# Performance work log

Measured on AMD Instinct MI355X. Metric: run time of the kernel, lower is better.

## Reference

```python
import jax, jax.numpy as jnp
import numpy as np

NTYPES = 2
B, N, MNEI = 4, 512, 100
M = MNEI * NTYPES          # neighbor slots = maxNeighborNum * ntypes
EMB_LAST = 100             # embedding net sizes [25, 50, 100]
FIT_H = 240
M2 = 16
RMIN, RMAX = 0.5, 6.0


def setup_inputs():
    key = jax.random.key(0)
    ks = jax.random.split(key, 24)
    r = jax.random.uniform(ks[0], (B, N, M), minval=0.6, maxval=7.0)
    v = jax.random.normal(ks[1], (B, N, M, 3))
    v = v / jnp.linalg.norm(v, axis=-1, keepdims=True)
    keep = jax.random.uniform(ks[2], (B, N, M)) < 0.7
    ImageDR = jnp.concatenate([r[..., None], r[..., None] * v], axis=-1)
    ImageDR = jnp.where(keep[..., None], ImageDR, 0.0).astype(jnp.float32)
    Imagetype_map = jax.random.randint(ks[3], (N,), 0, NTYPES)
    list_neigh = jax.random.randint(ks[4], (B, N, M), 0, N + 1)
    type_map = jnp.arange(NTYPES)
    davg = (0.01 * jax.random.normal(ks[5], (NTYPES, M, 4))).astype(jnp.float32)
    dstd = (1.0 + 0.1 * jax.random.uniform(ks[6], (NTYPES, M, 4))).astype(jnp.float32)

    def w(k, shape, fan):
        return (jax.random.normal(k, shape) / np.sqrt(fan)).astype(jnp.float32)

    def b(k, shape):
        return (0.1 * jax.random.normal(k, shape)).astype(jnp.float32)

    emb_W0 = w(ks[7], (NTYPES, NTYPES, 1, 25), 1)
    emb_b0 = b(ks[8], (NTYPES, NTYPES, 25))
    emb_W1 = w(ks[9], (NTYPES, NTYPES, 25, 50), 25)
    emb_b1 = b(ks[10], (NTYPES, NTYPES, 50))
    emb_W2 = w(ks[11], (NTYPES, NTYPES, 50, 100), 50)
    emb_b2 = b(ks[12], (NTYPES, NTYPES, 100))
    fin = M2 * EMB_LAST
    fit_W0 = w(ks[13], (NTYPES, fin, FIT_H), fin)
    fit_b0 = b(ks[14], (NTYPES, FIT_H))
    fit_W1 = w(ks[15], (NTYPES, FIT_H, FIT_H), FIT_H)
    fit_b1 = b(ks[16], (NTYPES, FIT_H))
    fit_W2 = w(ks[17], (NTYPES, FIT_H, FIT_H), FIT_H)
    fit_b2 = b(ks[18], (NTYPES, FIT_H))
    fit_W3 = w(ks[19], (NTYPES, FIT_H, 1), FIT_H)
    fit_b3 = b(ks[20], (NTYPES, 1))
    energy_shift = jnp.array([-3.37, -5.21], dtype=jnp.float32)
    return dict(list_neigh=list_neigh, Imagetype_map=Imagetype_map, type_map=type_map,
                ImageDR=ImageDR, nghost=0, davg=davg, dstd=dstd,
                emb_W0=emb_W0, emb_b0=emb_b0, emb_W1=emb_W1, emb_b1=emb_b1,
                emb_W2=emb_W2, emb_b2=emb_b2,
                fit_W0=fit_W0, fit_b0=fit_b0, fit_W1=fit_W1, fit_b1=fit_b1,
                fit_W2=fit_W2, fit_b2=fit_b2, fit_W3=fit_W3, fit_b3=fit_b3,
                energy_shift=energy_shift)


def _emb(s, W0, b0, W1, b1, W2, b2):
    # DeepPot-SE embedding net with doubling resnet connections
    h = jnp.tanh(s @ W0 + b0)                                   # [..., 25]
    h = jnp.tanh(h @ W1 + b1) + jnp.concatenate([h, h], -1)     # [..., 50]
    return jnp.tanh(h @ W2 + b2) + jnp.concatenate([h, h], -1)  # [..., 100]


def _fit(d, W0, b0, W1, b1, W2, b2, W3, b3):
    h = jnp.tanh(d @ W0 + b0)
    h = h + jnp.tanh(h @ W1 + b1)
    h = h + jnp.tanh(h @ W2 + b2)
    return h @ W3 + b3


def _forward(ImageDR, davg, dstd,
             emb_W0, emb_b0, emb_W1, emb_b1, emb_W2, emb_b2,
             fit_W0, fit_b0, fit_W1, fit_b1, fit_W2, fit_b2, fit_W3, fit_b3,
             energy_shift, Imagetype_map):
    Bsz, Nat, Mtot, _ = ImageDR.shape
    m = Mtot // NTYPES
    R = ImageDR[..., 0]
    Rsafe = jnp.where(R > 1e-5, R, 1.0)
    # smooth switching function s(r): 1/r below Rmin, polynomial taper to Rmax
    u = (R - RMIN) / (RMAX - RMIN)
    mid = (u ** 3 * (-6.0 * u * u + 15.0 * u - 10.0) + 1.0) / Rsafe
    S = jnp.where((R > 0) & (R < RMIN), 1.0 / Rsafe,
                  jnp.where((R > RMIN) & (R < RMAX), mid, 0.0))
    msk = (jnp.abs(R) > 1e-5)[..., None]
    Ri = jnp.concatenate([S[..., None],
                          jnp.where(msk, (S / Rsafe)[..., None] * ImageDR[..., 1:4], 0.0)],
                         axis=-1)                                    # [B,N,M,4] = (s, s*x/r, s*y/r, s*z/r)
    # per-center-type normalization (irregular gather of stats)
    Rn = (Ri - davg[Imagetype_map][None]) / dstd[Imagetype_map][None]
    tmask = [(Imagetype_map == i).astype(Rn.dtype)[None, :, None, None] for i in range(NTYPES)]
    xyz = jnp.zeros((Bsz, Nat, 4, EMB_LAST), Rn.dtype)
    for j in range(NTYPES):                                          # neighbor-type slice
        sl = Rn[:, :, j * m:(j + 1) * m, :]                          # [B,N,m,4]
        s = sl[..., 0:1]
        G = jnp.zeros(sl.shape[:3] + (EMB_LAST,), sl.dtype)
        for i in range(NTYPES):                                      # center type -> pair net (i, j)
            G = G + tmask[i] * _emb(s, emb_W0[i, j], emb_b0[i, j],
                                    emb_W1[i, j], emb_b1[i, j], emb_W2[i, j], emb_b2[i, j])
        xyz = xyz + jnp.einsum('bnmk,bnmc->bnkc', sl, G)
    xyz = xyz / (m * NTYPES)
    # descriptor D = (Ri^T G)^T (Ri^T G)[:, :M2], flattened -> [B,N,EMB_LAST*M2]
    D = jnp.einsum('bnkc,bnkd->bncd', xyz, xyz[..., :M2]).reshape(Bsz, Nat, -1)
    Ei = jnp.zeros((Bsz, Nat), D.dtype)
    for i in range(NTYPES):
        e = _fit(D, fit_W0[i], fit_b0[i], fit_W1[i], fit_b1[i],
                 fit_W2[i], fit_b2[i], fit_W3[i], fit_b3[i])[..., 0] + energy_shift[i]
        Ei = Ei + tmask[i][:, :, 0, 0] * e
    Etot = jnp.sum(Ei, axis=1)
    return Etot, Ei


def reference(list_neigh, Imagetype_map, type_map, ImageDR, nghost, davg, dstd,
              emb_W0, emb_b0, emb_W1, emb_b1, emb_W2, emb_b2,
              fit_W0, fit_b0, fit_W1, fit_b1, fit_W2, fit_b2, fit_W3, fit_b3,
              energy_shift):
    return _forward(ImageDR, davg, dstd,
                    emb_W0, emb_b0, emb_W1, emb_b1, emb_W2, emb_b2,
                    fit_W0, fit_b0, fit_W1, fit_b1, fit_W2, fit_b2, fit_W3, fit_b3,
                    energy_shift, Imagetype_map)
```

## Files before the change

kernel.cpp:

```cpp
#include <hip/hip_runtime.h>
#include <math.h>

#define NT 2
#define BSZ 4
#define NAT 512
#define NATOMS 2048
#define NNEI 200
#define EMB 100
#define FITH 240
#define DDIM 1600
#define TBK 1024

#define BIAS_F  16
#define W3C_F   (BIAS_F + 3 * 512)
#define PERM_I  2064
#define CNT_I   (PERM_I + 2048)
#define USH_BYTE 16512
#define TBL_U   0
#define W0T_U   409600
#define W1T_U   (W0T_U + 819200)
#define W2T_U   (W1T_U + 262144)
#define D_U     (W2T_U + 262144)
#define H0_U    (D_U + 3276800)
#define H1_U    (H0_U + 1048576)
#define USH_END (H1_U + 1048576)
#define WS_NEED ((size_t)USH_BYTE + (size_t)USH_END * 2)

#define N_W0 819200
#define N_W1 262144
#define N_W2 262144
#define N_B  1536
#define N_W3 512
#define N_EI 2048
#define N_WT (N_W0 + N_W1 + N_W2 + N_B + N_W3 + N_EI)
#define WT_BLK ((N_WT + 255) / 256)
#define TB_BLK 512

typedef short s8v __attribute__((ext_vector_type(8)));
typedef float f4v __attribute__((ext_vector_type(4)));

__device__ __forceinline__ float ftanh(float x) {
    float ax = fabsf(x);
    float e = __expf(2.0f * ax);
    float t = 1.0f - __fdividef(2.0f, e + 1.0f);
    return (x < 0.0f) ? -t : t;
}
__device__ __forceinline__ unsigned short f2bf(float f) {
    unsigned u = __float_as_uint(f);
    u += 0x7FFFu + ((u >> 16) & 1u);
    return (unsigned short)(u >> 16);
}
__device__ __forceinline__ float bf2f(unsigned short s) {
    return __uint_as_float(((unsigned)s) << 16);
}
__device__ __forceinline__ float calc_S(float R) {
    float Rsafe = (R > 1e-5f) ? R : 1.0f;
    float u = (R - 0.5f) * (1.0f / 5.5f);
    float uu = u * u;
    float mid = (u * uu * (-6.0f * uu + 15.0f * u - 10.0f) + 1.0f) / Rsafe;
    float S = 0.0f;
    if (R > 0.0f && R < 0.5f)      S = 1.0f / Rsafe;
    else if (R > 0.5f && R < 6.0f) S = mid;
    return S;
}

__global__ void __launch_bounds__(256) prep_kernel(
    const float* __restrict__ fW0, const float* __restrict__ fW1,
    const float* __restrict__ fW2,
    const float* __restrict__ fb0, const float* __restrict__ fb1,
    const float* __restrict__ fb2,
    const float* __restrict__ fW3, const float* __restrict__ fb3,
    const float* __restrict__ eshift,
    const float* __restrict__ davg, const float* __restrict__ dstd,
    const float* __restrict__ eW0, const float* __restrict__ eb0,
    const float* __restrict__ eW1, const float* __restrict__ eb1,
    const float* __restrict__ eW2, const float* __restrict__ eb2,
    const int* __restrict__ itype,
    float* __restrict__ ws, float* __restrict__ out)
{
    __shared__ float los[100], his[100];
    __shared__ float rng[2];
    __shared__ float h0s[8][25];
    __shared__ float h1s[8][50];
    __shared__ int pcnt, poff0, poff1;
    const int tid = threadIdx.x;
    int bxg = blockIdx.x;
    unsigned short* u0 = (unsigned short*)((char*)ws + USH_BYTE);

    if (bxg < WT_BLK) {
        int id = bxg * 256 + tid;
        if (id < N_W0) {
            int n = id / 1600, k = id - n * 1600;
            float v = 0.0f;
            if (n < 240)                  v = fW0[(size_t)k * 240 + n];
            else if (n >= 256 && n < 496) v = fW0[(size_t)(1600 + k) * 240 + (n - 256)];
            u0[W0T_U + id] = f2bf(v);
            return;
        }
        id -= N_W0;
        if (id < N_W1) {
            int n = id / 512, k = id - n * 512;
            float v = 0.0f;
            if (n < 240 && k < 240)       v = fW1[(size_t)k * 240 + n];
            else if (n >= 256 && n < 496 && k >= 256 && k < 496)
                                          v = fW1[(size_t)(240 + (k - 256)) * 240 + (n - 256)];
            u0[W1T_U + id] = f2bf(v);
            return;
        }
        id -= N_W1;
        if (id < N_W2) {
            int n = id / 512, k = id - n * 512;
            float v = 0.0f;
            if (n < 240 && k < 240)       v = fW2[(size_t)k * 240 + n];
            else if (n >= 256 && n < 496 && k >= 256 && k < 496)
                                          v = fW2[(size_t)(240 + (k - 256)) * 240 + (n - 256)];
            u0[W2T_U + id] = f2bf(v);
            return;
        }
        id -= N_W2;
        if (id < N_B) {
            int l = id / 512, n = id - l * 512;
            const float* fb = (l == 0) ? fb0 : (l == 1) ? fb1 : fb2;
            float v = 0.0f;
            if (n < 240)                  v = fb[n];
            else if (n >= 256 && n < 496) v = fb[240 + (n - 256)];
            ws[BIAS_F + l * 512 + n] = v;
            return;
        }
        id -= N_B;
        if (id < N_W3) {
            int n = id;
            float v = 0.0f;
            if (n < 240)                  v = fW3[n];
            else if (n >= 256 && n < 496) v = fW3[240 + (n - 256)];
            ws[W3C_F + n] = v;
            return;
        }
        id -= N_W3;
        if (id < N_EI) {
            int t = itype[id & (NAT - 1)];
            out[4 + id] = fb3[t] + eshift[t];
        }
        return;
    }
    bxg -= WT_BLK;
    if (bxg < TB_BLK) {
        const int nid = bxg >> 7;
        const int kb  = (bxg & 127) * 8;
        const int t = nid >> 1, j = nid & 1;
        if (tid < 100) {
            int m = j * 100 + tid;
            float av = davg[(t * NNEI + m) * 4];
            float sd = dstd[(t * NNEI + m) * 4];
            float inv = __fdividef(1.0f, sd);
            float a = (0.0f - av) * inv;
            float b = (2.0f - av) * inv;
            los[tid] = fminf(a, b);
            his[tid] = fmaxf(a, b);
        }
        __syncthreads();
        if (tid == 0) {
            float lo = los[0], hi = his[0];
            for (int i = 1; i < 100; ++i) { lo = fminf(lo, los[i]); hi = fmaxf(hi, his[i]); }
            rng[0] = lo; rng[1] = hi - lo;
            if (kb == 0) {
                ws[nid * 2] = lo;
                ws[nid * 2 + 1] = (float)(TBK - 1) / (hi - lo);
            }
        }
        __syncthreads();
        const float smin = rng[0], span = rng[1];
        const float* W0 = eW0 + nid * 25;
        const float* B0 = eb0 + nid * 25;
        if (tid < 200) {
            int q = tid / 25, a = tid % 25;
            float s = smin + span * ((float)(kb + q) * (1.0f / (TBK - 1)));
            h0s[q][a] = ftanh(fmaf(s, W0[a], B0[a]));
        }
        __syncthreads();
        const float* W1 = eW1 + nid * 1250;
        const float* B1 = eb1 + nid * 50;
        for (int idx = tid; idx < 400; idx += 256) {
            int q = idx / 50, cc = idx % 50;
            float acc = B1[cc];
#pragma unroll
            for (int a = 0; a < 25; ++a) acc = fmaf(h0s[q][a], W1[a * 50 + cc], acc);
            h1s[q][cc] = ftanh(acc) + h0s[q][(cc < 25) ? cc : cc - 25];
        }
        __syncthreads();
        const float* W2 = eW2 + nid * 5000;
        const float* B2 = eb2 + nid * 100;
        unsigned short* tblu = u0 + TBL_U;
        for (int idx = tid; idx < 800; idx += 256) {
            int q = idx / 100, c = idx % 100;
            float acc = B2[c];
#pragma unroll
            for (int a = 0; a < 50; ++a) acc = fmaf(h1s[q][a], W2[a * 100 + c], acc);
            float g = ftanh(acc) + h1s[q][(c < 50) ? c : c - 50];
            tblu[(size_t)(nid * TBK + kb + q) * 100 + c] = f2bf(g);
        }
        return;
    }
    if (tid == 0) { pcnt = 0; poff0 = 0; poff1 = 0; }
    __syncthreads();
    int* wsi = (int*)ws;
    int local0 = 0;
    for (int i = tid; i < NATOMS; i += 256) local0 += (itype[i & (NAT - 1)] == 0);
    atomicAdd(&pcnt, local0);
    __syncthreads();
    const int c0 = pcnt;
    for (int i = tid; i < NATOMS; i += 256) {
        int t = itype[i & (NAT - 1)];
        int pos = (t == 0) ? atomicAdd(&poff0, 1) : (c0 + atomicAdd(&poff1, 1));
        wsi[PERM_I + pos] = i;
    }
    if (tid == 0) { wsi[CNT_I] = c0; wsi[CNT_I + 1] = NATOMS - c0; }
}

__global__ void __launch_bounds__(128) embed_kernel(
    const int* __restrict__ itype, const float* __restrict__ imagedr,
    const float* __restrict__ davg, const float* __restrict__ dstd,
    float* __restrict__ ws)
{
    __shared__ __align__(16) float4 srn[NNEI];
    __shared__ float sx[NNEI];
    __shared__ float part[2][400];
    const int atom = blockIdx.x;
    const int n = atom & (NAT - 1);
    const int tid = threadIdx.x;
    const int t = itype[n];
    unsigned short* u0 = (unsigned short*)((char*)ws + USH_BYTE);

    const float sm0 = ws[(t * 2 + 0) * 2], sc0 = ws[(t * 2 + 0) * 2 + 1];
    const float sm1 = ws[(t * 2 + 1) * 2], sc1 = ws[(t * 2 + 1) * 2 + 1];

    for (int m = tid; m < NNEI; m += 128) {
        float4 dr = ((const float4*)imagedr)[(size_t)atom * NNEI + m];
        float R = dr.x;
        float S = calc_S(R);
        float Rsafe = (R > 1e-5f) ? R : 1.0f;
        float sr = (fabsf(R) > 1e-5f) ? (S / Rsafe) : 0.0f;
        float4 av = ((const float4*)davg)[t * NNEI + m];
        float4 sd = ((const float4*)dstd)[t * NNEI + m];
        float4 rv;
        rv.x = (S         - av.x) / sd.x;
        rv.y = (sr * dr.y - av.y) / sd.y;
        rv.z = (sr * dr.z - av.z) / sd.z;
        rv.w = (sr * dr.w - av.w) / sd.w;
        srn[m] = rv;
        float smin = (m >= 100) ? sm1 : sm0;
        float scal = (m >= 100) ? sc1 : sc0;
        sx[m] = fminf(fmaxf((rv.x - smin) * scal, 0.0f), (float)(TBK - 2) + 0.9999f);
    }
    __syncthreads();

    const int w = tid >> 6, lane = tid & 63;
    const unsigned short* T = u0 + TBL_U + (size_t)(t * 2 + w) * TBK * EMB;
    const bool hi = (lane < 36);
    float xA0 = 0, xA1 = 0, xA2 = 0, xA3 = 0;
    float xB0 = 0, xB1 = 0, xB2 = 0, xB3 = 0;
#pragma unroll 4
    for (int mi = 0; mi < 100; ++mi) {
        int m = w * 100 + mi;
        float4 rv = srn[m];
        float x = sx[m];
        int i = (int)x;
        float f = x - (float)i;
        const unsigned short* Tr = T + (size_t)i * EMB;
        float g0 = bf2f(Tr[lane]);
        float g1 = bf2f(Tr[EMB + lane]);
        float g = fmaf(f, g1 - g0, g0);
        xA0 = fmaf(rv.x, g, xA0); xA1 = fmaf(rv.y, g, xA1);
        xA2 = fmaf(rv.z, g, xA2); xA3 = fmaf(rv.w, g, xA3);
        if (hi) {
            float h0v = bf2f(Tr[64 + lane]);
            float h1v = bf2f(Tr[EMB + 64 + lane]);
            float g2 = fmaf(f, h1v - h0v, h0v);
            xB0 = fmaf(rv.x, g2, xB0); xB1 = fmaf(rv.y, g2, xB1);
            xB2 = fmaf(rv.z, g2, xB2); xB3 = fmaf(rv.w, g2, xB3);
        }
    }
    part[w][0 * 100 + lane] = xA0; part[w][1 * 100 + lane] = xA1;
    part[w][2 * 100 + lane] = xA2; part[w][3 * 100 + lane] = xA3;
    if (hi) {
        part[w][0 * 100 + 64 + lane] = xB0; part[w][1 * 100 + 64 + lane] = xB1;
        part[w][2 * 100 + 64 + lane] = xB2; part[w][3 * 100 + 64 + lane] = xB3;
    }
    __syncthreads();
    const float inv = 1.0f / 200.0f;
    for (int idx = tid; idx < 400; idx += 128)
        part[0][idx] = (part[0][idx] + part[1][idx]) * inv;
    __syncthreads();
    unsigned short* Drow = u0 + D_U + (size_t)atom * DDIM;
    const float* xt = part[0];
    for (int idx = tid; idx < DDIM; idx += 128) {
        int c = idx >> 4, d = idx & 15;
        float s = xt[c] * xt[d] + xt[100 + c] * xt[100 + d]
                + xt[200 + c] * xt[200 + d] + xt[300 + c] * xt[300 + d];
        Drow[idx] = f2bf(s);
    }
}

__global__ void __launch_bounds__(128) gemm0_kernel(
    const unsigned short* __restrict__ A,
    const unsigned short* __restrict__ BT,
    const float* __restrict__ bias,
    const int* __restrict__ wsi,
    unsigned short* __restrict__ Out)
{
    __shared__ float lred[64][17];
    const int z = blockIdx.z;
    const int cnt = wsi[CNT_I + z];
    const int my = blockIdx.y;
    if (my * 16 >= cnt) return;
    const int base = z ? wsi[CNT_I] : 0;
    const int tid = threadIdx.x;
    const int w = tid >> 6, lane = tid & 63;
    const int mr = lane & 15, q = lane >> 4;
    const int n0 = z * 256 + blockIdx.x * 64;
    const int m0 = my * 16;
    const int arow = wsi[PERM_I + base + min(m0 + mr, cnt - 1)];
    const unsigned short* Ap = A  + (size_t)arow * DDIM + w * 800 + q * 8;
    const unsigned short* Bp = BT + (size_t)(n0 + mr) * DDIM + w * 800 + q * 8;

    f4v a0 = {0,0,0,0}, a1 = {0,0,0,0}, a2 = {0,0,0,0}, a3 = {0,0,0,0};
#pragma unroll 5
    for (int kt = 0; kt < 25; ++kt) {
        s8v av = *(const s8v*)(Ap + kt * 32);
        s8v b0 = *(const s8v*)(Bp + kt * 32);
        s8v b1 = *(const s8v*)(Bp + 16 * DDIM + kt * 32);
        s8v b2 = *(const s8v*)(Bp + 32 * DDIM + kt * 32);
        s8v b3 = *(const s8v*)(Bp + 48 * DDIM + kt * 32);
        a0 = __builtin_amdgcn_mfma_f32_16x16x32_bf16(av, b0, a0, 0, 0, 0);
        a1 = __builtin_amdgcn_mfma_f32_16x16x32_bf16(av, b1, a1, 0, 0, 0);
        a2 = __builtin_amdgcn_mfma_f32_16x16x32_bf16(av, b2, a2, 0, 0, 0);
        a3 = __builtin_amdgcn_mfma_f32_16x16x32_bf16(av, b3, a3, 0, 0, 0);
    }
    if (w == 1) {
#pragma unroll
        for (int r = 0; r < 4; ++r) {
            lred[lane][r]      = a0[r];
            lred[lane][4 + r]  = a1[r];
            lred[lane][8 + r]  = a2[r];
            lred[lane][12 + r] = a3[r];
        }
    }
    __syncthreads();
    if (w == 0) {
#pragma unroll
        for (int j = 0; j < 4; ++j) {
            const int col = n0 + j * 16 + mr;
            const float bv = bias[col];
            f4v* ap = (j == 0) ? &a0 : (j == 1) ? &a1 : (j == 2) ? &a2 : &a3;
#pragma unroll
            for (int r = 0; r < 4; ++r) {
                int rl = m0 + q * 4 + r;
                if (rl < cnt) {
                    int orow = wsi[PERM_I + base + rl];
                    float s = (*ap)[r] + lred[lane][j * 4 + r] + bv;
                    Out[(size_t)orow * 512 + col] = f2bf(ftanh(s));
                }
            }
        }
    }
}

__global__ void __launch_bounds__(64) gemmr_kernel(
    const unsigned short* __restrict__ A, const unsigned short* __restrict__ BT,
    const float* __restrict__ bias, const unsigned short* __restrict__ Res,
    unsigned short* __restrict__ Out,
    const float* __restrict__ w3c, const int* __restrict__ wsi,
    float* __restrict__ out, int mode)
{
    const int z = blockIdx.z;
    const int cnt = wsi[CNT_I + z];
    const int my = blockIdx.y;
    if (my * 16 >= cnt) return;
    const int base = z ? wsi[CNT_I] : 0;
    const int lane = threadIdx.x;
    const int mr = lane & 15, q = lane >> 4;
    const int n0 = z * 256 + blockIdx.x * 64;
    const int k0 = z * 256;
    const int m0 = my * 16;
    const int arow = wsi[PERM_I + base + min(m0 + mr, cnt - 1)];
    const unsigned short* Ap = A  + (size_t)arow * 512 + k0 + q * 8;
    const unsigned short* Bp = BT + (size_t)(n0 + mr) * 512 + k0 + q * 8;

    f4v a0 = {0,0,0,0}, a1 = {0,0,0,0}, a2 = {0,0,0,0}, a3 = {0,0,0,0};
#pragma unroll
    for (int kt = 0; kt < 8; ++kt) {
        s8v av = *(const s8v*)(Ap + kt * 32);
        s8v b0 = *(const s8v*)(Bp + kt * 32);
        s8v b1 = *(const s8v*)(Bp + 16 * 512 + kt * 32);
        s8v b2 = *(const s8v*)(Bp + 32 * 512 + kt * 32);
        s8v b3 = *(const s8v*)(Bp + 48 * 512 + kt * 32);
        a0 = __builtin_amdgcn_mfma_f32_16x16x32_bf16(av, b0, a0, 0, 0, 0);
        a1 = __builtin_amdgcn_mfma_f32_16x16x32_bf16(av, b1, a1, 0, 0, 0);
        a2 = __builtin_amdgcn_mfma_f32_16x16x32_bf16(av, b2, a2, 0, 0, 0);
        a3 = __builtin_amdgcn_mfma_f32_16x16x32_bf16(av, b3, a3, 0, 0, 0);
    }
    const float bv0 = bias[n0 + mr],      bv1 = bias[n0 + 16 + mr];
    const float bv2 = bias[n0 + 32 + mr], bv3 = bias[n0 + 48 + mr];
    if (mode == 1) {
#pragma unroll
        for (int r = 0; r < 4; ++r) {
            int rl = m0 + q * 4 + r;
            if (rl < cnt) {
                int orow = wsi[PERM_I + base + rl];
                size_t b_ = (size_t)orow * 512 + n0 + mr;
                Out[b_]      = f2bf(bf2f(Res[b_])      + ftanh(a0[r] + bv0));
                Out[b_ + 16] = f2bf(bf2f(Res[b_ + 16]) + ftanh(a1[r] + bv1));
                Out[b_ + 32] = f2bf(bf2f(Res[b_ + 32]) + ftanh(a2[r] + bv2));
                Out[b_ + 48] = f2bf(bf2f(Res[b_ + 48]) + ftanh(a3[r] + bv3));
            }
        }
    } else {
        const float w30 = w3c[n0 + mr],      w31 = w3c[n0 + 16 + mr];
        const float w32 = w3c[n0 + 32 + mr], w33 = w3c[n0 + 48 + mr];
#pragma unroll
        for (int r = 0; r < 4; ++r) {
            int rl = m0 + q * 4 + r;
            if (rl < cnt) {
                int orow = wsi[PERM_I + base + rl];
                size_t b_ = (size_t)orow * 512 + n0 + mr;
                float p = (bf2f(Res[b_])      + ftanh(a0[r] + bv0)) * w30
                        + (bf2f(Res[b_ + 16]) + ftanh(a1[r] + bv1)) * w31
                        + (bf2f(Res[b_ + 32]) + ftanh(a2[r] + bv2)) * w32
                        + (bf2f(Res[b_ + 48]) + ftanh(a3[r] + bv3)) * w33;
                p += __shfl_xor(p, 1, 16);
                p += __shfl_xor(p, 2, 16);
                p += __shfl_xor(p, 4, 16);
                p += __shfl_xor(p, 8, 16);
                if (mr == 0) atomicAdd(&out[4 + orow], p);
            }
        }
    }
}

__global__ void etot_kernel(float* __restrict__ out) {
    const int b = blockIdx.x;
    float s = 0.0f;
    for (int n = threadIdx.x; n < NAT; n += 256) s += out[4 + b * NAT + n];
#pragma unroll
    for (int off = 32; off > 0; off >>= 1) s += __shfl_down(s, off, 64);
    __shared__ float rr[4];
    if ((threadIdx.x & 63) == 0) rr[threadIdx.x >> 6] = s;
    __syncthreads();
    if (threadIdx.x == 0) out[b] = rr[0] + rr[1] + rr[2] + rr[3];
}

__global__ void dp_atom_kernel(
    const int* __restrict__ itype, const float* __restrict__ imagedr,
    const float* __restrict__ davg, const float* __restrict__ dstd,
    const float* __restrict__ eW0, const float* __restrict__ eb0,
    const float* __restrict__ eW1, const float* __restrict__ eb1,
    const float* __restrict__ eW2, const float* __restrict__ eb2,
    const float* __restrict__ fW0, const float* __restrict__ fb0,
    const float* __restrict__ fW1, const float* __restrict__ fb1,
    const float* __restrict__ fW2, const float* __restrict__ fb2,
    const float* __restrict__ fW3, const float* __restrict__ fb3,
    const float* __restrict__ eshift, float* __restrict__ out)
{
    __shared__ __align__(16) float4 rn4[NNEI];
    __shared__ __align__(16) float  xyz[4 * EMB];
    __shared__ __align__(16) float  h0s[100 * 25];
    __shared__ __align__(16) float  smem[100 * 52];
    const int atom = blockIdx.x;
    const int n = atom & (NAT - 1);
    const int tid = threadIdx.x;
    const int t = itype[n];
    for (int m = tid; m < NNEI; m += 256) {
        float4 dr = ((const float4*)imagedr)[(size_t)atom * NNEI + m];
        float R = dr.x;
        float S = calc_S(R);
        float Rsafe = (R > 1e-5f) ? R : 1.0f;
        float sr = (fabsf(R) > 1e-5f) ? (S / Rsafe) : 0.0f;
        float4 av = ((const float4*)davg)[t * NNEI + m];
        float4 sd = ((const float4*)dstd)[t * NNEI + m];
        float4 rv;
        rv.x = (S - av.x) / sd.x; rv.y = (sr * dr.y - av.y) / sd.y;
        rv.z = (sr * dr.z - av.z) / sd.z; rv.w = (sr * dr.w - av.w) / sd.w;
        rn4[m] = rv;
    }
    const int c = tid & 127; const int mh = tid >> 7;
    float xp0 = 0, xp1 = 0, xp2 = 0, xp3 = 0;
    for (int j = 0; j < NT; ++j) {
        const int wb = t * NT + j;
        const float* W0 = eW0 + wb * 25; const float* B0 = eb0 + wb * 25;
        const float* W1 = eW1 + wb * 1250; const float* B1 = eb1 + wb * 50;
        const float* W2 = eW2 + wb * 5000; const float* B2 = eb2 + wb * 100;
        __syncthreads();
        for (int idx = tid; idx < 2500; idx += 256) {
            int m = idx / 25, a = idx - m * 25;
            h0s[idx] = ftanh(fmaf(rn4[j * 100 + m].x, W0[a], B0[a]));
        }
        __syncthreads();
        for (int idx = tid; idx < 5000; idx += 256) {
            int m = idx / 50, cc = idx - m * 50;
            const float* h0m = h0s + m * 25;
            float acc = B1[cc];
#pragma unroll
            for (int a = 0; a < 25; ++a) acc = fmaf(h0m[a], W1[a * 50 + cc], acc);
            smem[m * 52 + cc] = ftanh(acc) + h0m[(cc < 25) ? cc : cc - 25];
        }
        for (int idx = tid; idx < 200; idx += 256)
            smem[(idx >> 1) * 52 + 50 + (idx & 1)] = 0.0f;
        __syncthreads();
        if (c < EMB) {
            float w2c[52];
#pragma unroll
            for (int a = 0; a < 50; ++a) w2c[a] = W2[a * EMB + c];
            w2c[50] = 0; w2c[51] = 0;
            const float bc = B2[c];
            const int sk = (c < 50) ? c : c - 50;
            for (int i = 0; i < 50; ++i) {
                int m = mh * 50 + i;
                const float* h1m = smem + m * 52;
                float acc = bc;
#pragma unroll
                for (int q = 0; q < 13; ++q) {
                    float4 hv = ((const float4*)h1m)[q];
                    acc = fmaf(hv.x, w2c[4 * q], acc); acc = fmaf(hv.y, w2c[4 * q + 1], acc);
                    acc = fmaf(hv.z, w2c[4 * q + 2], acc); acc = fmaf(hv.w, w2c[4 * q + 3], acc);
                }
                float g = ftanh(acc) + h1m[sk];
                float4 rm = rn4[j * 100 + m];
                xp0 = fmaf(rm.x, g, xp0); xp1 = fmaf(rm.y, g, xp1);
                xp2 = fmaf(rm.z, g, xp2); xp3 = fmaf(rm.w, g, xp3);
            }
        }
    }
    __syncthreads();
    const float inv = 1.0f / 200.0f;
    if (mh == 0 && c < EMB) {
        xyz[c] = xp0 * inv; xyz[EMB + c] = xp1 * inv;
        xyz[2 * EMB + c] = xp2 * inv; xyz[3 * EMB + c] = xp3 * inv;
    }
    __syncthreads();
    if (mh == 1 && c < EMB) {
        xyz[c] += xp0 * inv; xyz[EMB + c] += xp1 * inv;
        xyz[2 * EMB + c] += xp2 * inv; xyz[3 * EMB + c] += xp3 * inv;
    }
    __syncthreads();
    float* Dld = smem;
    for (int idx = tid; idx < DDIM; idx += 256) {
        int cc = idx >> 4, d = idx & 15;
        Dld[idx] = xyz[cc] * xyz[d] + xyz[EMB + cc] * xyz[EMB + d]
                 + xyz[2 * EMB + cc] * xyz[2 * EMB + d] + xyz[3 * EMB + cc] * xyz[3 * EMB + d];
    }
    __syncthreads();
    float* hA = smem + DDIM; float* hB = hA + FITH; float* h2 = hB + FITH; float* red = h2 + FITH;
    if (tid < FITH) {
        const float* W = fW0 + (size_t)t * DDIM * FITH;
        float acc = fb0[t * FITH + tid];
        for (int f = 0; f < DDIM; f += 4) {
            float4 dv = *(const float4*)(Dld + f);
            acc = fmaf(dv.x, W[f * FITH + tid], acc); acc = fmaf(dv.y, W[(f + 1) * FITH + tid], acc);
            acc = fmaf(dv.z, W[(f + 2) * FITH + tid], acc); acc = fmaf(dv.w, W[(f + 3) * FITH + tid], acc);
        }
        hA[tid] = ftanh(acc);
    }
    __syncthreads();
    if (tid < FITH) {
        const float* W = fW1 + t * FITH * FITH;
        float acc = fb1[t * FITH + tid];
        for (int f = 0; f < FITH; f += 4) {
            float4 hv = *(const float4*)(hA + f);
            acc = fmaf(hv.x, W[f * FITH + tid], acc); acc = fmaf(hv.y, W[(f + 1) * FITH + tid], acc);
            acc = fmaf(hv.z, W[(f + 2) * FITH + tid], acc); acc = fmaf(hv.w, W[(f + 3) * FITH + tid], acc);
        }
        hB[tid] = hA[tid] + ftanh(acc);
    }
    __syncthreads();
    if (tid < FITH) {
        const float* W = fW2 + t * FITH * FITH;
        float acc = fb2[t * FITH + tid];
        for (int f = 0; f < FITH; f += 4) {
            float4 hv = *(const float4*)(hB + f);
            acc = fmaf(hv.x, W[f * FITH + tid], acc); acc = fmaf(hv.y, W[(f + 1) * FITH + tid], acc);
            acc = fmaf(hv.z, W[(f + 2) * FITH + tid], acc); acc = fmaf(hv.w, W[(f + 3) * FITH + tid], acc);
        }
        h2[tid] = hB[tid] + ftanh(acc);
    }
    __syncthreads();
    float p = (tid < FITH) ? h2[tid] * fW3[t * FITH + tid] : 0.0f;
#pragma unroll
    for (int off = 32; off > 0; off >>= 1) p += __shfl_down(p, off, 64);
    if ((tid & 63) == 0) red[tid >> 6] = p;
    __syncthreads();
    if (tid == 0) out[4 + atom] = red[0] + red[1] + red[2] + red[3] + fb3[t] + eshift[t];
}

extern "C" void kernel_launch(void* const* d_in, const int* in_sizes, int n_in,
                              void* d_out, int out_size, void* d_ws, size_t ws_size,
                              hipStream_t stream) {
    const int*   itype   = (const int*)  d_in[1];
    const float* imagedr = (const float*)d_in[3];
    const float* davg    = (const float*)d_in[5];
    const float* dstd    = (const float*)d_in[6];
    const float* eW0     = (const float*)d_in[7];
    const float* eb0     = (const float*)d_in[8];
    const float* eW1     = (const float*)d_in[9];
    const float* eb1     = (const float*)d_in[10];
    const float* eW2     = (const float*)d_in[11];
    const float* eb2     = (const float*)d_in[12];
    const float* fW0     = (const float*)d_in[13];
    const float* fb0     = (const float*)d_in[14];
    const float* fW1     = (const float*)d_in[15];
    const float* fb1     = (const float*)d_in[16];
    const float* fW2     = (const float*)d_in[17];
    const float* fb2     = (const float*)d_in[18];
    const float* fW3     = (const float*)d_in[19];
    const float* fb3     = (const float*)d_in[20];
    const float* eshift  = (const float*)d_in[21];
    float* out = (float*)d_out;
    float* ws  = (float*)d_ws;

    if (ws_size >= WS_NEED) {
        unsigned short* u0 = (unsigned short*)((char*)ws + USH_BYTE);
        const int* wsi = (const int*)ws;
        prep_kernel<<<WT_BLK + TB_BLK + 1, 256, 0, stream>>>(
            fW0, fW1, fW2, fb0, fb1, fb2, fW3, fb3, eshift,
            davg, dstd, eW0, eb0, eW1, eb1, eW2, eb2, itype, ws, out);
        embed_kernel<<<NATOMS, 128, 0, stream>>>(itype, imagedr, davg, dstd, ws);
        gemm0_kernel<<<dim3(4, 128, 2), 128, 0, stream>>>(
            u0 + D_U, u0 + W0T_U, ws + BIAS_F, wsi, u0 + H0_U);
        gemmr_kernel<<<dim3(4, 128, 2), 64, 0, stream>>>(
            u0 + H0_U, u0 + W1T_U, ws + BIAS_F + 512, u0 + H0_U, u0 + H1_U,
            nullptr, wsi, nullptr, 1);
        gemmr_kernel<<<dim3(4, 128, 2), 64, 0, stream>>>(
            u0 + H1_U, u0 + W2T_U, ws + BIAS_F + 1024, u0 + H1_U, nullptr,
            ws + W3C_F, wsi, out, 2);
        etot_kernel<<<BSZ, 256, 0, stream>>>(out);
    } else {
        dp_atom_kernel<<<NATOMS, 256, 0, stream>>>(itype, imagedr, davg, dstd,
            eW0, eb0, eW1, eb1, eW2, eb2,
            fW0, fb0, fW1, fb1, fW2, fb2, fW3, fb3, eshift, out);
        etot_kernel<<<BSZ, 256, 0, stream>>>(out);
    }
}
```

Before: 191.4 us.

## Fuse three fitting-net GEMM kernels into one kernel with LDS-resident hidden activations

Replaces the gemm0 kernel and the two gemmr launches with a single fit_kernel. Each 512-thread block owns 16 atom rows and all 256 output columns of its type, and keeps the hidden activations in padded shared memory between layers. This removes two kernel launches, the global-memory round trips for H0/H1, and the atomicAdd on energies, which become one plain add per row. In exchange each layer's K is split across two wave halves, which adds block-wide syncs and LDS reductions, and the grid shrinks to 256 blocks, so parallelism drops.

```diff
diff --git a/kernel.cpp b/kernel.cpp
--- a/kernel.cpp
+++ b/kernel.cpp
@@ -35,6 +35,8 @@
 #define N_WT (N_W0 + N_W1 + N_W2 + N_B + N_W3 + N_EI)
 #define WT_BLK ((N_WT + 255) / 256)
 #define TB_BLK 512
+
+#define HPAD 264
 
 typedef short s8v __attribute__((ext_vector_type(8)));
 typedef float f4v __attribute__((ext_vector_type(4)));
@@ -301,138 +303,159 @@
     }
 }
 
-__global__ void __launch_bounds__(128) gemm0_kernel(
+__device__ __forceinline__ void fit_gemm256(
+    const unsigned short* Hsrc, const unsigned short* Bp,
+    int h, int mr, int q, f4v acc[4])
+{
+#pragma unroll
+    for (int kt = 0; kt < 4; ++kt) {
+        s8v av = *(const s8v*)((const char*)Hsrc
+                 + (size_t)mr * (HPAD * 2) + h * 256 + q * 16 + kt * 64);
+#pragma unroll
+        for (int j = 0; j < 4; ++j) {
+            s8v b = *(const s8v*)(Bp + j * 16 * 512 + kt * 32);
+            acc[j] = __builtin_amdgcn_mfma_f32_16x16x32_bf16(av, b, acc[j], 0, 0, 0);
+        }
+    }
+}
+
+__global__ void __launch_bounds__(512) fit_kernel(
     const unsigned short* __restrict__ A,
-    const unsigned short* __restrict__ BT,
-    const float* __restrict__ bias,
+    const unsigned short* __restrict__ W0T,
+    const unsigned short* __restrict__ W1T,
+    const unsigned short* __restrict__ W2T,
+    const float* __restrict__ biases,
+    const float* __restrict__ w3c,
     const int* __restrict__ wsi,
-    unsigned short* __restrict__ Out)
+    float* __restrict__ out)
 {
-    __shared__ float lred[64][17];
-    const int z = blockIdx.z;
+    __shared__ float lred[4][64][17];
+    __shared__ unsigned short Hs0[16 * HPAD];
+    __shared__ unsigned short Hs1[16 * HPAD];
+    __shared__ float red2[16][4];
+
+    const int z = blockIdx.y;
     const int cnt = wsi[CNT_I + z];
-    const int my = blockIdx.y;
+    const int my = blockIdx.x;
     if (my * 16 >= cnt) return;
     const int base = z ? wsi[CNT_I] : 0;
     const int tid = threadIdx.x;
     const int w = tid >> 6, lane = tid & 63;
     const int mr = lane & 15, q = lane >> 4;
-    const int n0 = z * 256 + blockIdx.x * 64;
+    const int wc = w & 3, h = w >> 2;
+    const int n0 = z * 256 + wc * 64;
     const int m0 = my * 16;
     const int arow = wsi[PERM_I + base + min(m0 + mr, cnt - 1)];
-    const unsigned short* Ap = A  + (size_t)arow * DDIM + w * 800 + q * 8;
-    const unsigned short* Bp = BT + (size_t)(n0 + mr) * DDIM + w * 800 + q * 8;
-
-    f4v a0 = {0,0,0,0}, a1 = {0,0,0,0}, a2 = {0,0,0,0}, a3 = {0,0,0,0};
+
+    {
+        const unsigned short* Ap = A   + (size_t)arow * DDIM + h * 800 + q * 8;
+        const unsigned short* Bp = W0T + (size_t)(n0 + mr) * DDIM + h * 800 + q * 8;
+        f4v a0 = {0,0,0,0}, a1 = {0,0,0,0}, a2 = {0,0,0,0}, a3 = {0,0,0,0};
 #pragma unroll 5
-    for (int kt = 0; kt < 25; ++kt) {
-        s8v av = *(const s8v*)(Ap + kt * 32);
-        s8v b0 = *(const s8v*)(Bp + kt * 32);
-        s8v b1 = *(const s8v*)(Bp + 16 * DDIM + kt * 32);
-        s8v b2 = *(const s8v*)(Bp + 32 * DDIM + kt * 32);
-        s8v b3 = *(const s8v*)(Bp + 48 * DDIM + kt * 32);
-        a0 = __builtin_amdgcn_mfma_f32_16x16x32_bf16(av, b0, a0, 0, 0, 0);
-        a1 = __builtin_amdgcn_mfma_f32_16x16x32_bf16(av, b1, a1, 0, 0, 0);
-        a2 = __builtin_amdgcn_mfma_f32_16x16x32_bf16(av, b2, a2, 0, 0, 0);
-        a3 = __builtin_amdgcn_mfma_f32_16x16x32_bf16(av, b3, a3, 0, 0, 0);
-    }
-    if (w == 1) {
-#pragma unroll
-        for (int r = 0; r < 4; ++r) {
-            lred[lane][r]      = a0[r];
-            lred[lane][4 + r]  = a1[r];
-            lred[lane][8 + r]  = a2[r];
-            lred[lane][12 + r] = a3[r];
-        }
-    }
-    __syncthreads();
-    if (w == 0) {
-#pragma unroll
-        for (int j = 0; j < 4; ++j) {
-            const int col = n0 + j * 16 + mr;
-            const float bv = bias[col];
-            f4v* ap = (j == 0) ? &a0 : (j == 1) ? &a1 : (j == 2) ? &a2 : &a3;
+        for (int kt = 0; kt < 25; ++kt) {
+            s8v av = *(const s8v*)(Ap + kt * 32);
+            s8v b0 = *(const s8v*)(Bp + kt * 32);
+            s8v b1 = *(const s8v*)(Bp + 16 * DDIM + kt * 32);
+            s8v b2 = *(const s8v*)(Bp + 32 * DDIM + kt * 32);
+            s8v b3 = *(const s8v*)(Bp + 48 * DDIM + kt * 32);
+            a0 = __builtin_amdgcn_mfma_f32_16x16x32_bf16(av, b0, a0, 0, 0, 0);
+            a1 = __builtin_amdgcn_mfma_f32_16x16x32_bf16(av, b1, a1, 0, 0, 0);
+            a2 = __builtin_amdgcn_mfma_f32_16x16x32_bf16(av, b2, a2, 0, 0, 0);
+            a3 = __builtin_amdgcn_mfma_f32_16x16x32_bf16(av, b3, a3, 0, 0, 0);
+        }
+        if (h == 1) {
 #pragma unroll
             for (int r = 0; r < 4; ++r) {
-                int rl = m0 + q * 4 + r;
-                if (rl < cnt) {
-                    int orow = wsi[PERM_I + base + rl];
-                    float s = (*ap)[r] + lred[lane][j * 4 + r] + bv;
-                    Out[(size_t)orow * 512 + col] = f2bf(ftanh(s));
+                lred[wc][lane][r]      = a0[r];
+                lred[wc][lane][4 + r]  = a1[r];
+                lred[wc][lane][8 + r]  = a2[r];
+                lred[wc][lane][12 + r] = a3[r];
+            }
+        }
+        __syncthreads();
+        if (h == 0) {
+#pragma unroll
+            for (int j = 0; j < 4; ++j) {
+                const float bv = biases[n0 + j * 16 + mr];
+                f4v* ap = (j == 0) ? &a0 : (j == 1) ? &a1 : (j == 2) ? &a2 : &a3;
+#pragma unroll
+                for (int r = 0; r < 4; ++r) {
+                    float s = (*ap)[r] + lred[wc][lane][j * 4 + r] + bv;
+                    int row = q * 4 + r, col = wc * 64 + j * 16 + mr;
+                    Hs0[row * HPAD + col] = f2bf(ftanh(s));
                 }
             }
         }
-    }
-}
-
-__global__ void __launch_bounds__(64) gemmr_kernel(
-    const unsigned short* __restrict__ A, const unsigned short* __restrict__ BT,
-    const float* __restrict__ bias, const unsigned short* __restrict__ Res,
-    unsigned short* __restrict__ Out,
-    const float* __restrict__ w3c, const int* __restrict__ wsi,
-    float* __restrict__ out, int mode)
-{
-    const int z = blockIdx.z;
-    const int cnt = wsi[CNT_I + z];
-    const int my = blockIdx.y;
-    if (my * 16 >= cnt) return;
-    const int base = z ? wsi[CNT_I] : 0;
-    const int lane = threadIdx.x;
-    const int mr = lane & 15, q = lane >> 4;
-    const int n0 = z * 256 + blockIdx.x * 64;
-    const int k0 = z * 256;
-    const int m0 = my * 16;
-    const int arow = wsi[PERM_I + base + min(m0 + mr, cnt - 1)];
-    const unsigned short* Ap = A  + (size_t)arow * 512 + k0 + q * 8;
-    const unsigned short* Bp = BT + (size_t)(n0 + mr) * 512 + k0 + q * 8;
-
-    f4v a0 = {0,0,0,0}, a1 = {0,0,0,0}, a2 = {0,0,0,0}, a3 = {0,0,0,0};
-#pragma unroll
-    for (int kt = 0; kt < 8; ++kt) {
-        s8v av = *(const s8v*)(Ap + kt * 32);
-        s8v b0 = *(const s8v*)(Bp + kt * 32);
-        s8v b1 = *(const s8v*)(Bp + 16 * 512 + kt * 32);
-        s8v b2 = *(const s8v*)(Bp + 32 * 512 + kt * 32);
-        s8v b3 = *(const s8v*)(Bp + 48 * 512 + kt * 32);
-        a0 = __builtin_amdgcn_mfma_f32_16x16x32_bf16(av, b0, a0, 0, 0, 0);
-        a1 = __builtin_amdgcn_mfma_f32_16x16x32_bf16(av, b1, a1, 0, 0, 0);
-        a2 = __builtin_amdgcn_mfma_f32_16x16x32_bf16(av, b2, a2, 0, 0, 0);
-        a3 = __builtin_amdgcn_mfma_f32_16x16x32_bf16(av, b3, a3, 0, 0, 0);
-    }
-    const float bv0 = bias[n0 + mr],      bv1 = bias[n0 + 16 + mr];
-    const float bv2 = bias[n0 + 32 + mr], bv3 = bias[n0 + 48 + mr];
-    if (mode == 1) {
-#pragma unroll
-        for (int r = 0; r < 4; ++r) {
-            int rl = m0 + q * 4 + r;
-            if (rl < cnt) {
-                int orow = wsi[PERM_I + base + rl];
-                size_t b_ = (size_t)orow * 512 + n0 + mr;
-                Out[b_]      = f2bf(bf2f(Res[b_])      + ftanh(a0[r] + bv0));
-                Out[b_ + 16] = f2bf(bf2f(Res[b_ + 16]) + ftanh(a1[r] + bv1));
-                Out[b_ + 32] = f2bf(bf2f(Res[b_ + 32]) + ftanh(a2[r] + bv2));
-                Out[b_ + 48] = f2bf(bf2f(Res[b_ + 48]) + ftanh(a3[r] + bv3));
+        __syncthreads();
+    }
+
+    {
+        const unsigned short* Bp = W1T + (size_t)(n0 + mr) * 512 + z * 256 + h * 128 + q * 8;
+        f4v acc[4] = {{0,0,0,0},{0,0,0,0},{0,0,0,0},{0,0,0,0}};
+        fit_gemm256(Hs0, Bp, h, mr, q, acc);
+        if (h == 1) {
+#pragma unroll
+            for (int j = 0; j < 4; ++j)
+#pragma unroll
+                for (int r = 0; r < 4; ++r) lred[wc][lane][j * 4 + r] = acc[j][r];
+        }
+        __syncthreads();
+        if (h == 0) {
+#pragma unroll
+            for (int j = 0; j < 4; ++j) {
+                const float bv = biases[512 + n0 + j * 16 + mr];
+#pragma unroll
+                for (int r = 0; r < 4; ++r) {
+                    float s = acc[j][r] + lred[wc][lane][j * 4 + r] + bv;
+                    int row = q * 4 + r, col = wc * 64 + j * 16 + mr;
+                    float hv = bf2f(Hs0[row * HPAD + col]) + ftanh(s);
+                    Hs1[row * HPAD + col] = f2bf(hv);
+                }
             }
         }
-    } else {
-        const float w30 = w3c[n0 + mr],      w31 = w3c[n0 + 16 + mr];
-        const float w32 = w3c[n0 + 32 + mr], w33 = w3c[n0 + 48 + mr];
-#pragma unroll
-        for (int r = 0; r < 4; ++r) {
-            int rl = m0 + q * 4 + r;
-            if (rl < cnt) {
-                int orow = wsi[PERM_I + base + rl];
-                size_t b_ = (size_t)orow * 512 + n0 + mr;
-                float p = (bf2f(Res[b_])      + ftanh(a0[r] + bv0)) * w30
-                        + (bf2f(Res[b_ + 16]) + ftanh(a1[r] + bv1)) * w31
-                        + (bf2f(Res[b_ + 32]) + ftanh(a2[r] + bv2)) * w32
-                        + (bf2f(Res[b_ + 48]) + ftanh(a3[r] + bv3)) * w33;
+        __syncthreads();
+    }
+
+    {
+        const unsigned short* Bp = W2T + (size_t)(n0 + mr) * 512 + z * 256 + h * 128 + q * 8;
+        f4v acc[4] = {{0,0,0,0},{0,0,0,0},{0,0,0,0},{0,0,0,0}};
+        fit_gemm256(Hs1, Bp, h, mr, q, acc);
+        if (h == 1) {
+#pragma unroll
+            for (int j = 0; j < 4; ++j)
+#pragma unroll
+                for (int r = 0; r < 4; ++r) lred[wc][lane][j * 4 + r] = acc[j][r];
+        }
+        __syncthreads();
+        if (h == 0) {
+            float pr[4] = {0, 0, 0, 0};
+#pragma unroll
+            for (int j = 0; j < 4; ++j) {
+                const int col = n0 + j * 16 + mr;
+                const float bv = biases[1024 + col];
+                const float wv = w3c[col];
+#pragma unroll
+                for (int r = 0; r < 4; ++r) {
+                    float s = acc[j][r] + lred[wc][lane][j * 4 + r] + bv;
+                    int row = q * 4 + r, coll = wc * 64 + j * 16 + mr;
+                    float hv = bf2f(Hs1[row * HPAD + coll]) + ftanh(s);
+                    pr[r] = fmaf(hv, wv, pr[r]);
+                }
+            }
+#pragma unroll
+            for (int r = 0; r < 4; ++r) {
+                float p = pr[r];
                 p += __shfl_xor(p, 1, 16);
                 p += __shfl_xor(p, 2, 16);
                 p += __shfl_xor(p, 4, 16);
                 p += __shfl_xor(p, 8, 16);
-                if (mr == 0) atomicAdd(&out[4 + orow], p);
+                if (mr == 0) red2[q * 4 + r][wc] = p;
             }
+        }
+        __syncthreads();
+        if (tid < 16 && m0 + tid < cnt) {
+            const int orow = wsi[PERM_I + base + m0 + tid];
+            out[4 + orow] += red2[tid][0] + red2[tid][1] + red2[tid][2] + red2[tid][3];
         }
     }
 }
@@ -623,14 +646,9 @@
             fW0, fW1, fW2, fb0, fb1, fb2, fW3, fb3, eshift,
             davg, dstd, eW0, eb0, eW1, eb1, eW2, eb2, itype, ws, out);
         embed_kernel<<<NATOMS, 128, 0, stream>>>(itype, imagedr, davg, dstd, ws);
-        gemm0_kernel<<<dim3(4, 128, 2), 128, 0, stream>>>(
-            u0 + D_U, u0 + W0T_U, ws + BIAS_F, wsi, u0 + H0_U);
-        gemmr_kernel<<<dim3(4, 128, 2), 64, 0, stream>>>(
-            u0 + H0_U, u0 + W1T_U, ws + BIAS_F + 512, u0 + H0_U, u0 + H1_U,
-            nullptr, wsi, nullptr, 1);
-        gemmr_kernel<<<dim3(4, 128, 2), 64, 0, stream>>>(
-            u0 + H1_U, u0 + W2T_U, ws + BIAS_F + 1024, u0 + H1_U, nullptr,
-            ws + W3C_F, wsi, out, 2);
+        fit_kernel<<<dim3(128, 2), 512, 0, stream>>>(
+            u0 + D_U, u0 + W0T_U, u0 + W1T_U, u0 + W2T_U,
+            ws + BIAS_F, ws + W3C_F, wsi, out);
         etot_kernel<<<BSZ, 256, 0, stream>>>(out);
     } else {
         dp_atom_kernel<<<NATOMS, 256, 0, stream>>>(itype, imagedr, davg, dstd,
```

Result: no change. 193.7 us (+1.2%).
